# Performance work log

Measured on AMD Instinct MI355X. Metric: run time of the kernel, lower is better.

## Reference

```python
import jax, jax.numpy as jnp
import numpy as np

N_NODES = 50000
MUL_S = 256   # 0e multiplicity
MUL_V = 128   # 1o multiplicity
# combined coefficients: e3nn path_weight sqrt((2l_out+1)/fan_in) * CG normalization
C_000 = 1.0 / np.sqrt(256.0)            # 0e x 0e -> 0e
C_011 = 1.0 / np.sqrt(128.0)            # 0e x 1o -> 1o  (sqrt(3/128) * 1/sqrt(3))
C_101 = 1.0 / np.sqrt(256.0)            # 1o x 0e -> 1o
C_110 = 1.0 / np.sqrt(384.0)            # 1o x 1o -> 0e  (sqrt(1/128) * 1/sqrt(3))
C_111 = 1.0 / 16.0                      # 1o x 1o -> 1e  (sqrt(3/128) * 1/sqrt(6))

_e = np.zeros((3, 3, 3), dtype=np.float32)
_e[0, 1, 2] = _e[1, 2, 0] = _e[2, 0, 1] = 1.0
_e[0, 2, 1] = _e[2, 1, 0] = _e[1, 0, 2] = -1.0
EPS = jnp.asarray(_e)


def setup_inputs() -> dict:
    key = jax.random.key(0)
    ks = jax.random.split(key, 9)
    return {
        "node_feat": jax.random.normal(ks[0], (N_NODES, MUL_S + 3 * MUL_V), jnp.float32),
        # TensorProduct 'uvu' internal weights, one (mul_u, mul_v) matrix per path
        "w_00_0": jax.random.normal(ks[1], (MUL_S, MUL_S), jnp.float32),
        "w_01_1": jax.random.normal(ks[2], (MUL_S, MUL_V), jnp.float32),
        "w_10_1": jax.random.normal(ks[3], (MUL_V, MUL_S), jnp.float32),
        "w_11_0": jax.random.normal(ks[4], (MUL_V, MUL_V), jnp.float32),
        "w_11_1": jax.random.normal(ks[5], (MUL_V, MUL_V), jnp.float32),
        # o3.Linear weights per output irrep (fan_in, mul_out)
        "W_0e": jax.random.normal(ks[6], (MUL_S + MUL_V, MUL_S), jnp.float32),
        "W_1o": jax.random.normal(ks[7], (MUL_S + MUL_V, MUL_V), jnp.float32),
        "W_1e": jax.random.normal(ks[8], (MUL_V, MUL_V), jnp.float32),
    }


def reference(node_feat, w_00_0, w_01_1, w_10_1, w_11_0, w_11_1, W_0e, W_1o, W_1e):
    N = node_feat.shape[0]
    s = node_feat[:, :MUL_S]                                   # [N, 256]   0e
    v = node_feat[:, MUL_S:].reshape(N, MUL_V, 3)              # [N, 128, 3] 1o

    # TensorProduct paths ('uvu': out mul = mul of input-1 channel u)
    p1 = C_000 * jnp.einsum('uv,zu,zv->zu', w_00_0, s, s)          # [N,256] 0e
    p2 = C_011 * jnp.einsum('uv,zu,zvj->zuj', w_01_1, s, v)        # [N,256,3] 1o
    p3 = C_101 * jnp.einsum('uv,zuj,zv->zuj', w_10_1, v, s)        # [N,128,3] 1o
    p4 = C_110 * jnp.einsum('uv,zuj,zvj->zu', w_11_0, v, v)        # [N,128] 0e
    p5 = C_111 * jnp.einsum('uv,ijk,zui,zvj->zuk', w_11_1, EPS, v, v)  # [N,128,3] 1e

    # o3.Linear (irrep-wise mixing, 1/sqrt(fan_in) normalization)
    tp_0e = jnp.concatenate([p1, p4], axis=1)                      # [N, 384]
    tp_1o = jnp.concatenate([p2, p3], axis=1)                      # [N, 384, 3]
    out_0e = (tp_0e @ W_0e) / jnp.sqrt(384.0)                      # [N, 256]
    out_1o = jnp.einsum('zuj,uo->zoj', tp_1o, W_1o) / jnp.sqrt(384.0)  # [N,128,3]
    out_1e = jnp.einsum('zuj,uo->zoj', p5, W_1e) / jnp.sqrt(128.0)     # [N,128,3]

    return jnp.concatenate(
        [out_0e, out_1o.reshape(N, -1), out_1e.reshape(N, -1)], axis=1
    )  # [N, 1024] = 256x0e + 128x1o + 128x1e
```

## Files before the change

kernel.cpp:

```cpp
#include <hip/hip_runtime.h>

typedef _Float16 f16;
typedef _Float16 f16x8 __attribute__((ext_vector_type(8)));
typedef _Float16 f16x4 __attribute__((ext_vector_type(4)));
typedef float f32x4 __attribute__((ext_vector_type(4)));

#define MFMA16(a, b, c) __builtin_amdgcn_mfma_f32_16x16x32_f16(a, b, c, 0, 0, 0)

__device__ __forceinline__ void pack_one(int local, const float* __restrict__ src,
                                         f16* __restrict__ dst, int K, int R, int transpose) {
    int i = local & 7;
    int l = (local >> 3) & 63;
    int p = local >> 9;
    int rt16 = R >> 4;
    int rb = p % rt16;
    int kb = p / rt16;
    int k = kb * 32 + ((l >> 4) << 3) + i;
    int r = rb * 16 + (l & 15);
    float v = transpose ? src[k * R + r] : src[r * K + k];
    dst[local] = (f16)v;
}

__global__ void pack_weights(const float* __restrict__ w00, const float* __restrict__ w01,
                             const float* __restrict__ w10, const float* __restrict__ w110,
                             const float* __restrict__ w111, const float* __restrict__ W0e,
                             const float* __restrict__ W1o, const float* __restrict__ W1e,
                             f16* __restrict__ dst) {
    int idx = blockIdx.x * 256 + threadIdx.x;
    if (idx < 65536)        pack_one(idx,          w00,  dst,          256, 256, 0);
    else if (idx < 98304)   pack_one(idx - 65536,  w01,  dst + 65536,  128, 256, 0);
    else if (idx < 131072)  pack_one(idx - 98304,  w10,  dst + 98304,  256, 128, 0);
    else if (idx < 147456)  pack_one(idx - 131072, w110, dst + 131072, 128, 128, 0);
    else if (idx < 163840)  pack_one(idx - 147456, w111, dst + 147456, 128, 128, 0);
    else if (idx < 262144)  pack_one(idx - 163840, W0e,  dst + 163840, 384, 256, 1);
    else if (idx < 311296)  pack_one(idx - 262144, W1o,  dst + 262144, 384, 128, 1);
    else                    pack_one(idx - 311296, W1e,  dst + 311296, 128, 128, 1);
}

#define NT 32
#define S16B   0
#define VBASE(j) (16384 + (j) * 8192)
#define TB     40960
#define A3B    65536
#define MBASE(j) (TB + (j) * 8192)
#define P5BASE(j) ((j) == 0 ? A3B : (S16B + ((j) - 1) * 8192))
#define LDS_BYTES 73728

__device__ __forceinline__ f16x8 afrag(const unsigned char* lds, int base, int pitchh,
                                       int row0, int k0, int lr, int lg) {
    int row = row0 + lr;
    int off = base + row * (pitchh * 2) + (((k0 + (lg << 3)) * 2) ^ ((row & 7) << 4));
    return *(const f16x8*)(lds + off);
}
__device__ __forceinline__ f16x4 ldsv4(const unsigned char* lds, int base, int pitchh,
                                       int row, int col) {
    int off = base + row * (pitchh * 2) + ((col * 2) ^ ((row & 7) << 4));
    return *(const f16x4*)(lds + off);
}
__device__ __forceinline__ void stsv4(unsigned char* lds, int base, int pitchh,
                                      int row, int col, f16x4 v) {
    int off = base + row * (pitchh * 2) + ((col * 2) ^ ((row & 7) << 4));
    *(f16x4*)(lds + off) = v;
}
__device__ __forceinline__ void ldss(unsigned char* lds, int base, int pitchh,
                                     int row, int col, float v) {
    int off = base + row * (pitchh * 2) + ((col * 2) ^ ((row & 7) << 4));
    *(f16*)(lds + off) = (f16)v;
}
__device__ __forceinline__ f16x8 wfrag(const f16* __restrict__ panel, int rt16, int kb,
                                       int rb, int lane) {
    return *(const f16x8*)(panel + (size_t)((kb * rt16 + rb) * 512 + lane * 8));
}

__global__ __launch_bounds__(512, 2)
void node_tp(const float* __restrict__ nf, const f16* __restrict__ wp,
             float* __restrict__ out, int n_nodes) {
    __shared__ __align__(16) unsigned char lds[LDS_BYTES];
    const int tid = threadIdx.x;
    const int lane = tid & 63;
    const int wv = tid >> 6;
    const int z0 = blockIdx.x * NT;
    const int nvalid = min(NT, n_nodes - z0);
    const int lr = lane & 15;
    const int lg = lane >> 4;
    const int ng = wv >> 2;
    const int wr = wv & 3;

    const f16* w00p  = wp;
    const f16* w01p  = wp + 65536;
    const f16* w10p  = wp + 98304;
    const f16* w110p = wp + 131072;
    const f16* w111p = wp + 147456;
    const f16* W0ep  = wp + 163840;
    const f16* W1op  = wp + 262144;
    const f16* W1ep  = wp + 311296;

    const float C000 = 0.0625f;
    const float C011 = 0.08838834764831843f;
    const float C101 = 0.0625f;
    const float C110 = 0.05103103630798287f;
    const float C111 = 0.0625f;
    const float RS384 = 0.05103103630798287f;
    const float RS128 = 0.08838834764831843f;

    #pragma unroll 5
    for (int q = tid; q < NT * 160; q += 512) {
        int row = q / 160;
        int c4 = q - row * 160;
        float4 v4 = make_float4(0.f, 0.f, 0.f, 0.f);
        if (row < nvalid)
            v4 = ((const float4*)(nf + (size_t)(z0 + row) * 640))[c4];
        int c = c4 * 4;
        if (c < 256) {
            f16x4 h = {(f16)v4.x, (f16)v4.y, (f16)v4.z, (f16)v4.w};
            int off = S16B + row * 512 + ((c * 2) ^ ((row & 7) << 4));
            *(f16x4*)(lds + off) = h;
        } else {
            float vv[4] = {v4.x, v4.y, v4.z, v4.w};
            #pragma unroll
            for (int e = 0; e < 4; ++e) {
                int m = c - 256 + e;
                int u = m / 3;
                int j = m - u * 3;
                ldss(lds, VBASE(j), 128, row, u, vv[e]);
            }
        }
    }
    __syncthreads();

    {
        f32x4 acc[2][2] = {};
        f16x8 a0 = wfrag(w00p, 16, 0, 2 * wv, lane);
        f16x8 a1 = wfrag(w00p, 16, 0, 2 * wv + 1, lane);
        #pragma unroll 1
        for (int ks = 0; ks < 8; ++ks) {
            int kn = ks + 1 < 8 ? ks + 1 : ks;
            f16x8 n0 = wfrag(w00p, 16, kn, 2 * wv, lane);
            f16x8 n1 = wfrag(w00p, 16, kn, 2 * wv + 1, lane);
            #pragma unroll
            for (int nt = 0; nt < 2; ++nt) {
                f16x8 b = afrag(lds, S16B, 256, nt * 16, ks * 32, lr, lg);
                acc[0][nt] = MFMA16(a0, b, acc[0][nt]);
                acc[1][nt] = MFMA16(a1, b, acc[1][nt]);
            }
            a0 = n0; a1 = n1;
        }
        #pragma unroll
        for (int rt = 0; rt < 2; ++rt)
            #pragma unroll
            for (int nt = 0; nt < 2; ++nt) {
                int node = nt * 16 + lr;
                int u0 = wv * 32 + rt * 16 + lg * 4;
                f16x4 s4 = ldsv4(lds, S16B, 256, node, u0);
                f16x4 t4;
                #pragma unroll
                for (int r = 0; r < 4; ++r)
                    t4[r] = (f16)(C000 * (float)s4[r] * acc[rt][nt][r]);
                stsv4(lds, TB, 384, node, u0, t4);
            }
    }
    {
        f32x4 acc[3][2] = {};
        #pragma unroll
        for (int ks = 0; ks < 4; ++ks) {
            f16x8 a0 = wfrag(w110p, 8, ks, 2 * wr, lane);
            f16x8 a1 = wfrag(w110p, 8, ks, 2 * wr + 1, lane);
            #pragma unroll
            for (int j = 0; j < 3; ++j) {
                f16x8 b = afrag(lds, VBASE(j), 128, ng * 16, ks * 32, lr, lg);
                acc[j][0] = MFMA16(a0, b, acc[j][0]);
                acc[j][1] = MFMA16(a1, b, acc[j][1]);
            }
        }
        #pragma unroll
        for (int r2 = 0; r2 < 2; ++r2) {
            int node = ng * 16 + lr;
            int u0 = (2 * wr + r2) * 16 + lg * 4;
            float p4[4] = {0.f, 0.f, 0.f, 0.f};
            #pragma unroll
            for (int j = 0; j < 3; ++j) {
                f16x4 v4 = ldsv4(lds, VBASE(j), 128, node, u0);
                #pragma unroll
                for (int r = 0; r < 4; ++r)
                    p4[r] += (float)v4[r] * acc[j][r2][r];
            }
            f16x4 t4;
            #pragma unroll
            for (int r = 0; r < 4; ++r) t4[r] = (f16)(C110 * p4[r]);
            stsv4(lds, TB, 384, node, 256 + u0, t4);
        }
    }
    __syncthreads();

    {
        f32x4 acc[2][2] = {};
        f16x8 a0 = wfrag(W0ep, 16, 0, 2 * wv, lane);
        f16x8 a1 = wfrag(W0ep, 16, 0, 2 * wv + 1, lane);
        #pragma unroll 1
        for (int ks = 0; ks < 12; ++ks) {
            int kn = ks + 1 < 12 ? ks + 1 : ks;
            f16x8 n0 = wfrag(W0ep, 16, kn, 2 * wv, lane);
            f16x8 n1 = wfrag(W0ep, 16, kn, 2 * wv + 1, lane);
            #pragma unroll
            for (int nt = 0; nt < 2; ++nt) {
                f16x8 b = afrag(lds, TB, 384, nt * 16, ks * 32, lr, lg);
                acc[0][nt] = MFMA16(a0, b, acc[0][nt]);
                acc[1][nt] = MFMA16(a1, b, acc[1][nt]);
            }
            a0 = n0; a1 = n1;
        }
        #pragma unroll
        for (int rt = 0; rt < 2; ++rt)
            #pragma unroll
            for (int nt = 0; nt < 2; ++nt) {
                int node = nt * 16 + lr;
                if (node < nvalid) {
                    int o = wv * 32 + rt * 16 + lg * 4;
                    float4 o4;
                    o4.x = RS384 * acc[rt][nt][0];
                    o4.y = RS384 * acc[rt][nt][1];
                    o4.z = RS384 * acc[rt][nt][2];
                    o4.w = RS384 * acc[rt][nt][3];
                    *(float4*)(&out[(size_t)(z0 + node) * 1024 + o]) = o4;
                }
            }
    }
    {
        f32x4 acc[2] = {};
        f16x8 a0 = wfrag(w10p, 8, 0, 2 * wr, lane);
        f16x8 a1 = wfrag(w10p, 8, 0, 2 * wr + 1, lane);
        #pragma unroll 1
        for (int ks = 0; ks < 8; ++ks) {
            int kn = ks + 1 < 8 ? ks + 1 : ks;
            f16x8 n0 = wfrag(w10p, 8, kn, 2 * wr, lane);
            f16x8 n1 = wfrag(w10p, 8, kn, 2 * wr + 1, lane);
            f16x8 b = afrag(lds, S16B, 256, ng * 16, ks * 32, lr, lg);
            acc[0] = MFMA16(a0, b, acc[0]);
            acc[1] = MFMA16(a1, b, acc[1]);
            a0 = n0; a1 = n1;
        }
        #pragma unroll
        for (int r2 = 0; r2 < 2; ++r2) {
            int node = ng * 16 + lr;
            f16x4 t4;
            #pragma unroll
            for (int r = 0; r < 4; ++r) t4[r] = (f16)acc[r2][r];
            stsv4(lds, A3B, 128, node, (2 * wr + r2) * 16 + lg * 4, t4);
        }
    }
    __syncthreads();

    f32x4 acc1o[2][3] = {};
    #pragma unroll
    for (int j = 0; j < 3; ++j) {
        {
            f32x4 a2[2][2] = {};
            #pragma unroll
            for (int ks = 0; ks < 4; ++ks) {
                f16x8 a0 = wfrag(w01p, 16, ks, 2 * wv, lane);
                f16x8 a1 = wfrag(w01p, 16, ks, 2 * wv + 1, lane);
                #pragma unroll
                for (int nt = 0; nt < 2; ++nt) {
                    f16x8 b = afrag(lds, VBASE(j), 128, nt * 16, ks * 32, lr, lg);
                    a2[0][nt] = MFMA16(a0, b, a2[0][nt]);
                    a2[1][nt] = MFMA16(a1, b, a2[1][nt]);
                }
            }
            #pragma unroll
            for (int rt = 0; rt < 2; ++rt)
                #pragma unroll
                for (int nt = 0; nt < 2; ++nt) {
                    int node = nt * 16 + lr;
                    int u0 = wv * 32 + rt * 16 + lg * 4;
                    f16x4 s4 = ldsv4(lds, S16B, 256, node, u0);
                    f16x4 t4;
                    #pragma unroll
                    for (int r = 0; r < 4; ++r)
                        t4[r] = (f16)(C011 * (float)s4[r] * a2[rt][nt][r]);
                    stsv4(lds, TB, 384, node, u0, t4);
                }
        }
        #pragma unroll 1
        for (int q = tid; q < NT * 32; q += 512) {
            int row = q >> 5;
            int col = (q & 31) * 4;
            f16x4 v4 = ldsv4(lds, VBASE(j), 128, row, col);
            f16x4 a34 = ldsv4(lds, A3B, 128, row, col);
            f16x4 t4;
            #pragma unroll
            for (int r = 0; r < 4; ++r)
                t4[r] = (f16)(C101 * (float)v4[r] * (float)a34[r]);
            stsv4(lds, TB, 384, row, 256 + col, t4);
        }
        __syncthreads();
        {
            f16x8 a0 = wfrag(W1op, 8, 0, 2 * wr, lane);
            f16x8 a1 = wfrag(W1op, 8, 0, 2 * wr + 1, lane);
            #pragma unroll 1
            for (int ks = 0; ks < 12; ++ks) {
                int kn = ks + 1 < 12 ? ks + 1 : ks;
                f16x8 n0 = wfrag(W1op, 8, kn, 2 * wr, lane);
                f16x8 n1 = wfrag(W1op, 8, kn, 2 * wr + 1, lane);
                f16x8 b = afrag(lds, TB, 384, ng * 16, ks * 32, lr, lg);
                acc1o[0][j] = MFMA16(a0, b, acc1o[0][j]);
                acc1o[1][j] = MFMA16(a1, b, acc1o[1][j]);
                a0 = n0; a1 = n1;
            }
        }
        __syncthreads();
    }
    #pragma unroll
    for (int r2 = 0; r2 < 2; ++r2) {
        int node = ng * 16 + lr;
        if (node < nvalid) {
            int o0 = (2 * wr + r2) * 16 + lg * 4;
            float vals[12];
            #pragma unroll
            for (int r = 0; r < 4; ++r)
                #pragma unroll
                for (int j = 0; j < 3; ++j)
                    vals[r * 3 + j] = RS384 * acc1o[r2][j][r];
            size_t base = (size_t)(z0 + node) * 1024 + 256 + 3 * o0;
            #pragma unroll
            for (int qq = 0; qq < 3; ++qq) {
                float4 f;
                f.x = vals[qq * 4 + 0]; f.y = vals[qq * 4 + 1];
                f.z = vals[qq * 4 + 2]; f.w = vals[qq * 4 + 3];
                *(float4*)(&out[base + qq * 4]) = f;
            }
        }
    }

    #pragma unroll 1
    for (int j = 0; j < 3; ++j) {
        f32x4 am[2] = {};
        #pragma unroll
        for (int ks = 0; ks < 4; ++ks) {
            f16x8 a0 = wfrag(w111p, 8, ks, 2 * wr, lane);
            f16x8 a1 = wfrag(w111p, 8, ks, 2 * wr + 1, lane);
            f16x8 b = afrag(lds, VBASE(j), 128, ng * 16, ks * 32, lr, lg);
            am[0] = MFMA16(a0, b, am[0]);
            am[1] = MFMA16(a1, b, am[1]);
        }
        #pragma unroll
        for (int r2 = 0; r2 < 2; ++r2) {
            int node = ng * 16 + lr;
            f16x4 t4;
            #pragma unroll
            for (int r = 0; r < 4; ++r) t4[r] = (f16)am[r2][r];
            stsv4(lds, MBASE(j), 128, node, (2 * wr + r2) * 16 + lg * 4, t4);
        }
    }
    __syncthreads();
    #pragma unroll 1
    for (int q = tid; q < NT * 32; q += 512) {
        int row = q >> 5;
        int col = (q & 31) * 4;
        f16x4 v0 = ldsv4(lds, VBASE(0), 128, row, col);
        f16x4 v1 = ldsv4(lds, VBASE(1), 128, row, col);
        f16x4 v2 = ldsv4(lds, VBASE(2), 128, row, col);
        f16x4 m0 = ldsv4(lds, MBASE(0), 128, row, col);
        f16x4 m1 = ldsv4(lds, MBASE(1), 128, row, col);
        f16x4 m2 = ldsv4(lds, MBASE(2), 128, row, col);
        f16x4 c0, c1, c2;
        #pragma unroll
        for (int r = 0; r < 4; ++r) {
            c0[r] = (f16)(C111 * ((float)v1[r] * (float)m2[r] - (float)v2[r] * (float)m1[r]));
            c1[r] = (f16)(C111 * ((float)v2[r] * (float)m0[r] - (float)v0[r] * (float)m2[r]));
            c2[r] = (f16)(C111 * ((float)v0[r] * (float)m1[r] - (float)v1[r] * (float)m0[r]));
        }
        stsv4(lds, P5BASE(0), 128, row, col, c0);
        stsv4(lds, P5BASE(1), 128, row, col, c1);
        stsv4(lds, P5BASE(2), 128, row, col, c2);
    }
    __syncthreads();

    {
        f32x4 acc[2][3] = {};
        #pragma unroll
        for (int j = 0; j < 3; ++j)
            #pragma unroll
            for (int ks = 0; ks < 4; ++ks) {
                f16x8 a0 = wfrag(W1ep, 8, ks, 2 * wr, lane);
                f16x8 a1 = wfrag(W1ep, 8, ks, 2 * wr + 1, lane);
                f16x8 b = afrag(lds, P5BASE(j), 128, ng * 16, ks * 32, lr, lg);
                acc[0][j] = MFMA16(a0, b, acc[0][j]);
                acc[1][j] = MFMA16(a1, b, acc[1][j]);
            }
        #pragma unroll
        for (int r2 = 0; r2 < 2; ++r2) {
            int node = ng * 16 + lr;
            if (node < nvalid) {
                int o0 = (2 * wr + r2) * 16 + lg * 4;
                float vals[12];
                #pragma unroll
                for (int r = 0; r < 4; ++r)
                    #pragma unroll
                    for (int j = 0; j < 3; ++j)
                        vals[r * 3 + j] = RS128 * acc[r2][j][r];
                size_t base = (size_t)(z0 + node) * 1024 + 640 + 3 * o0;
                #pragma unroll
                for (int qq = 0; qq < 3; ++qq) {
                    float4 f;
                    f.x = vals[qq * 4 + 0]; f.y = vals[qq * 4 + 1];
                    f.z = vals[qq * 4 + 2]; f.w = vals[qq * 4 + 3];
                    *(float4*)(&out[base + qq * 4]) = f;
                }
            }
        }
    }
}

extern "C" void kernel_launch(void* const* d_in, const int* in_sizes, int n_in,
                              void* d_out, int out_size, void* d_ws, size_t ws_size,
                              hipStream_t stream) {
    const float* nf   = (const float*)d_in[0];
    const float* w00  = (const float*)d_in[1];
    const float* w01  = (const float*)d_in[2];
    const float* w10  = (const float*)d_in[3];
    const float* w110 = (const float*)d_in[4];
    const float* w111 = (const float*)d_in[5];
    const float* W0e  = (const float*)d_in[6];
    const float* W1o  = (const float*)d_in[7];
    const float* W1e  = (const float*)d_in[8];
    f16* wpack = (f16*)d_ws;

    int n_nodes = in_sizes[0] / 640;
    pack_weights<<<1280, 256, 0, stream>>>(w00, w01, w10, w110, w111, W0e, W1o, W1e, wpack);
    int blocks = (n_nodes + NT - 1) / NT;
    node_tp<<<blocks, 512, 0, stream>>>(nf, wpack, (float*)d_out, n_nodes);
}
```

Before: 194.2 us.

## Fuse w00/w10 GEMMs, keep scalar tiles in registers, shrink LDS footprint

```diff
diff --git a/kernel.cpp b/kernel.cpp
--- a/kernel.cpp
+++ b/kernel.cpp
@@ -38,13 +38,11 @@
 }
 
 #define NT 32
-#define S16B   0
-#define VBASE(j) (16384 + (j) * 8192)
-#define TB     40960
-#define A3B    65536
-#define MBASE(j) (TB + (j) * 8192)
-#define P5BASE(j) ((j) == 0 ? A3B : (S16B + ((j) - 1) * 8192))
-#define LDS_BYTES 73728
+#define ST     0
+#define VB(j)  (16384 + (j) * 8192)
+#define T2B    40960
+#define MB(j)  ((j) == 2 ? T2B : (ST + (j) * 8192))
+#define LDS_BYTES 49152
 
 __device__ __forceinline__ f16x8 afrag(const unsigned char* lds, int base, int pitchh,
                                        int row0, int k0, int lr, int lg) {
@@ -113,7 +111,7 @@
         int c = c4 * 4;
         if (c < 256) {
             f16x4 h = {(f16)v4.x, (f16)v4.y, (f16)v4.z, (f16)v4.w};
-            int off = S16B + row * 512 + ((c * 2) ^ ((row & 7) << 4));
+            int off = ST + row * 512 + ((c * 2) ^ ((row & 7) << 4));
             *(f16x4*)(lds + off) = h;
         } else {
             float vv[4] = {v4.x, v4.y, v4.z, v4.w};
@@ -122,92 +120,97 @@
                 int m = c - 256 + e;
                 int u = m / 3;
                 int j = m - u * 3;
-                ldss(lds, VBASE(j), 128, row, u, vv[e]);
-            }
-        }
-    }
+                ldss(lds, VB(j), 128, row, u, vv[e]);
+            }
+        }
+    }
+    f16x4 s4r[2][2];
+    #pragma unroll
+    for (int rt = 0; rt < 2; ++rt)
+        #pragma unroll
+        for (int nt = 0; nt < 2; ++nt) {
+            int node = nt * 16 + lr;
+            float4 f = make_float4(0.f, 0.f, 0.f, 0.f);
+            if (node < nvalid)
+                f = *(const float4*)(nf + (size_t)(z0 + node) * 640 + wv * 32 + rt * 16 + lg * 4);
+            s4r[rt][nt] = f16x4{(f16)f.x, (f16)f.y, (f16)f.z, (f16)f.w};
+        }
+    __syncthreads();
+
+    f32x4 acc1[2][2] = {};
+    f32x4 acc3[2] = {};
+    {
+        #pragma unroll
+        for (int ks = 0; ks < 8; ++ks) {
+            f16x8 a0 = wfrag(w00p, 16, ks, 2 * wv, lane);
+            f16x8 a1 = wfrag(w00p, 16, ks, 2 * wv + 1, lane);
+            f16x8 g0 = wfrag(w10p, 8, ks, 2 * wr, lane);
+            f16x8 g1 = wfrag(w10p, 8, ks, 2 * wr + 1, lane);
+            f16x8 b0 = afrag(lds, ST, 256, 0, ks * 32, lr, lg);
+            f16x8 b1 = afrag(lds, ST, 256, 16, ks * 32, lr, lg);
+            acc1[0][0] = MFMA16(a0, b0, acc1[0][0]);
+            acc1[0][1] = MFMA16(a0, b1, acc1[0][1]);
+            acc1[1][0] = MFMA16(a1, b0, acc1[1][0]);
+            acc1[1][1] = MFMA16(a1, b1, acc1[1][1]);
+            f16x8 bg = ng ? b1 : b0;
+            acc3[0] = MFMA16(g0, bg, acc3[0]);
+            acc3[1] = MFMA16(g1, bg, acc3[1]);
+        }
+        f32x4 p4p[2] = {};
+        #pragma unroll
+        for (int j = 0; j < 3; ++j) {
+            f32x4 a4[2] = {};
+            #pragma unroll
+            for (int ks = 0; ks < 4; ++ks) {
+                f16x8 h0 = wfrag(w110p, 8, ks, 2 * wr, lane);
+                f16x8 h1 = wfrag(w110p, 8, ks, 2 * wr + 1, lane);
+                f16x8 b = afrag(lds, VB(j), 128, ng * 16, ks * 32, lr, lg);
+                a4[0] = MFMA16(h0, b, a4[0]);
+                a4[1] = MFMA16(h1, b, a4[1]);
+            }
+            #pragma unroll
+            for (int r2 = 0; r2 < 2; ++r2) {
+                f16x4 v4 = ldsv4(lds, VB(j), 128, ng * 16 + lr, (2 * wr + r2) * 16 + lg * 4);
+                #pragma unroll
+                for (int r = 0; r < 4; ++r)
+                    p4p[r2][r] += (float)v4[r] * a4[r2][r];
+            }
+        }
+        #pragma unroll
+        for (int r2 = 0; r2 < 2; ++r2) {
+            f16x4 t4;
+            #pragma unroll
+            for (int r = 0; r < 4; ++r) t4[r] = (f16)(C110 * p4p[r2][r]);
+            stsv4(lds, T2B, 128, ng * 16 + lr, (2 * wr + r2) * 16 + lg * 4, t4);
+        }
+    }
+    __syncthreads();
+
+    #pragma unroll
+    for (int rt = 0; rt < 2; ++rt)
+        #pragma unroll
+        for (int nt = 0; nt < 2; ++nt) {
+            f16x4 t4;
+            #pragma unroll
+            for (int r = 0; r < 4; ++r)
+                t4[r] = (f16)(C000 * (float)s4r[rt][nt][r] * acc1[rt][nt][r]);
+            stsv4(lds, ST, 256, nt * 16 + lr, wv * 32 + rt * 16 + lg * 4, t4);
+        }
     __syncthreads();
 
     {
         f32x4 acc[2][2] = {};
-        f16x8 a0 = wfrag(w00p, 16, 0, 2 * wv, lane);
-        f16x8 a1 = wfrag(w00p, 16, 0, 2 * wv + 1, lane);
-        #pragma unroll 1
-        for (int ks = 0; ks < 8; ++ks) {
-            int kn = ks + 1 < 8 ? ks + 1 : ks;
-            f16x8 n0 = wfrag(w00p, 16, kn, 2 * wv, lane);
-            f16x8 n1 = wfrag(w00p, 16, kn, 2 * wv + 1, lane);
+        #pragma unroll
+        for (int ks = 0; ks < 12; ++ks) {
+            f16x8 a0 = wfrag(W0ep, 16, ks, 2 * wv, lane);
+            f16x8 a1 = wfrag(W0ep, 16, ks, 2 * wv + 1, lane);
             #pragma unroll
             for (int nt = 0; nt < 2; ++nt) {
-                f16x8 b = afrag(lds, S16B, 256, nt * 16, ks * 32, lr, lg);
+                f16x8 b = (ks < 8) ? afrag(lds, ST, 256, nt * 16, ks * 32, lr, lg)
+                                   : afrag(lds, T2B, 128, nt * 16, (ks - 8) * 32, lr, lg);
                 acc[0][nt] = MFMA16(a0, b, acc[0][nt]);
                 acc[1][nt] = MFMA16(a1, b, acc[1][nt]);
             }
-            a0 = n0; a1 = n1;
-        }
-        #pragma unroll
-        for (int rt = 0; rt < 2; ++rt)
-            #pragma unroll
-            for (int nt = 0; nt < 2; ++nt) {
-                int node = nt * 16 + lr;
-                int u0 = wv * 32 + rt * 16 + lg * 4;
-                f16x4 s4 = ldsv4(lds, S16B, 256, node, u0);
-                f16x4 t4;
-                #pragma unroll
-                for (int r = 0; r < 4; ++r)
-                    t4[r] = (f16)(C000 * (float)s4[r] * acc[rt][nt][r]);
-                stsv4(lds, TB, 384, node, u0, t4);
-            }
-    }
-    {
-        f32x4 acc[3][2] = {};
-        #pragma unroll
-        for (int ks = 0; ks < 4; ++ks) {
-            f16x8 a0 = wfrag(w110p, 8, ks, 2 * wr, lane);
-            f16x8 a1 = wfrag(w110p, 8, ks, 2 * wr + 1, lane);
-            #pragma unroll
-            for (int j = 0; j < 3; ++j) {
-                f16x8 b = afrag(lds, VBASE(j), 128, ng * 16, ks * 32, lr, lg);
-                acc[j][0] = MFMA16(a0, b, acc[j][0]);
-                acc[j][1] = MFMA16(a1, b, acc[j][1]);
-            }
-        }
-        #pragma unroll
-        for (int r2 = 0; r2 < 2; ++r2) {
-            int node = ng * 16 + lr;
-            int u0 = (2 * wr + r2) * 16 + lg * 4;
-            float p4[4] = {0.f, 0.f, 0.f, 0.f};
-            #pragma unroll
-            for (int j = 0; j < 3; ++j) {
-                f16x4 v4 = ldsv4(lds, VBASE(j), 128, node, u0);
-                #pragma unroll
-                for (int r = 0; r < 4; ++r)
-                    p4[r] += (float)v4[r] * acc[j][r2][r];
-            }
-            f16x4 t4;
-            #pragma unroll
-            for (int r = 0; r < 4; ++r) t4[r] = (f16)(C110 * p4[r]);
-            stsv4(lds, TB, 384, node, 256 + u0, t4);
-        }
-    }
-    __syncthreads();
-
-    {
-        f32x4 acc[2][2] = {};
-        f16x8 a0 = wfrag(W0ep, 16, 0, 2 * wv, lane);
-        f16x8 a1 = wfrag(W0ep, 16, 0, 2 * wv + 1, lane);
-        #pragma unroll 1
-        for (int ks = 0; ks < 12; ++ks) {
-            int kn = ks + 1 < 12 ? ks + 1 : ks;
-            f16x8 n0 = wfrag(W0ep, 16, kn, 2 * wv, lane);
-            f16x8 n1 = wfrag(W0ep, 16, kn, 2 * wv + 1, lane);
-            #pragma unroll
-            for (int nt = 0; nt < 2; ++nt) {
-                f16x8 b = afrag(lds, TB, 384, nt * 16, ks * 32, lr, lg);
-                acc[0][nt] = MFMA16(a0, b, acc[0][nt]);
-                acc[1][nt] = MFMA16(a1, b, acc[1][nt]);
-            }
-            a0 = n0; a1 = n1;
         }
         #pragma unroll
         for (int rt = 0; rt < 2; ++rt)
@@ -225,90 +228,55 @@
                 }
             }
     }
-    {
-        f32x4 acc[2] = {};
-        f16x8 a0 = wfrag(w10p, 8, 0, 2 * wr, lane);
-        f16x8 a1 = wfrag(w10p, 8, 0, 2 * wr + 1, lane);
-        #pragma unroll 1
-        for (int ks = 0; ks < 8; ++ks) {
-            int kn = ks + 1 < 8 ? ks + 1 : ks;
-            f16x8 n0 = wfrag(w10p, 8, kn, 2 * wr, lane);
-            f16x8 n1 = wfrag(w10p, 8, kn, 2 * wr + 1, lane);
-            f16x8 b = afrag(lds, S16B, 256, ng * 16, ks * 32, lr, lg);
-            acc[0] = MFMA16(a0, b, acc[0]);
-            acc[1] = MFMA16(a1, b, acc[1]);
-            a0 = n0; a1 = n1;
-        }
-        #pragma unroll
-        for (int r2 = 0; r2 < 2; ++r2) {
-            int node = ng * 16 + lr;
-            f16x4 t4;
-            #pragma unroll
-            for (int r = 0; r < 4; ++r) t4[r] = (f16)acc[r2][r];
-            stsv4(lds, A3B, 128, node, (2 * wr + r2) * 16 + lg * 4, t4);
-        }
-    }
-    __syncthreads();
 
     f32x4 acc1o[2][3] = {};
     #pragma unroll
     for (int j = 0; j < 3; ++j) {
-        {
-            f32x4 a2[2][2] = {};
-            #pragma unroll
-            for (int ks = 0; ks < 4; ++ks) {
-                f16x8 a0 = wfrag(w01p, 16, ks, 2 * wv, lane);
-                f16x8 a1 = wfrag(w01p, 16, ks, 2 * wv + 1, lane);
+        f32x4 acc2[2][2] = {};
+        #pragma unroll
+        for (int ks = 0; ks < 4; ++ks) {
+            f16x8 a0 = wfrag(w01p, 16, ks, 2 * wv, lane);
+            f16x8 a1 = wfrag(w01p, 16, ks, 2 * wv + 1, lane);
+            #pragma unroll
+            for (int nt = 0; nt < 2; ++nt) {
+                f16x8 b = afrag(lds, VB(j), 128, nt * 16, ks * 32, lr, lg);
+                acc2[0][nt] = MFMA16(a0, b, acc2[0][nt]);
+                acc2[1][nt] = MFMA16(a1, b, acc2[1][nt]);
+            }
+        }
+        __syncthreads();
+        #pragma unroll
+        for (int rt = 0; rt < 2; ++rt)
+            #pragma unroll
+            for (int nt = 0; nt < 2; ++nt) {
+                f16x4 t4;
                 #pragma unroll
-                for (int nt = 0; nt < 2; ++nt) {
-                    f16x8 b = afrag(lds, VBASE(j), 128, nt * 16, ks * 32, lr, lg);
-                    a2[0][nt] = MFMA16(a0, b, a2[0][nt]);
-                    a2[1][nt] = MFMA16(a1, b, a2[1][nt]);
-                }
-            }
-            #pragma unroll
-            for (int rt = 0; rt < 2; ++rt)
-                #pragma unroll
-                for (int nt = 0; nt < 2; ++nt) {
-                    int node = nt * 16 + lr;
-                    int u0 = wv * 32 + rt * 16 + lg * 4;
-                    f16x4 s4 = ldsv4(lds, S16B, 256, node, u0);
-                    f16x4 t4;
-                    #pragma unroll
-                    for (int r = 0; r < 4; ++r)
-                        t4[r] = (f16)(C011 * (float)s4[r] * a2[rt][nt][r]);
-                    stsv4(lds, TB, 384, node, u0, t4);
-                }
-        }
-        #pragma unroll 1
-        for (int q = tid; q < NT * 32; q += 512) {
-            int row = q >> 5;
-            int col = (q & 31) * 4;
-            f16x4 v4 = ldsv4(lds, VBASE(j), 128, row, col);
-            f16x4 a34 = ldsv4(lds, A3B, 128, row, col);
+                for (int r = 0; r < 4; ++r)
+                    t4[r] = (f16)(C011 * (float)s4r[rt][nt][r] * acc2[rt][nt][r]);
+                stsv4(lds, ST, 256, nt * 16 + lr, wv * 32 + rt * 16 + lg * 4, t4);
+            }
+        #pragma unroll
+        for (int r2 = 0; r2 < 2; ++r2) {
+            f16x4 v4 = ldsv4(lds, VB(j), 128, ng * 16 + lr, (2 * wr + r2) * 16 + lg * 4);
             f16x4 t4;
             #pragma unroll
             for (int r = 0; r < 4; ++r)
-                t4[r] = (f16)(C101 * (float)v4[r] * (float)a34[r]);
-            stsv4(lds, TB, 384, row, 256 + col, t4);
+                t4[r] = (f16)(C101 * (float)v4[r] * acc3[r2][r]);
+            stsv4(lds, T2B, 128, ng * 16 + lr, (2 * wr + r2) * 16 + lg * 4, t4);
         }
         __syncthreads();
-        {
-            f16x8 a0 = wfrag(W1op, 8, 0, 2 * wr, lane);
-            f16x8 a1 = wfrag(W1op, 8, 0, 2 * wr + 1, lane);
-            #pragma unroll 1
-            for (int ks = 0; ks < 12; ++ks) {
-                int kn = ks + 1 < 12 ? ks + 1 : ks;
-                f16x8 n0 = wfrag(W1op, 8, kn, 2 * wr, lane);
-                f16x8 n1 = wfrag(W1op, 8, kn, 2 * wr + 1, lane);
-                f16x8 b = afrag(lds, TB, 384, ng * 16, ks * 32, lr, lg);
-                acc1o[0][j] = MFMA16(a0, b, acc1o[0][j]);
-                acc1o[1][j] = MFMA16(a1, b, acc1o[1][j]);
-                a0 = n0; a1 = n1;
-            }
-        }
-        __syncthreads();
-    }
+        #pragma unroll
+        for (int ks = 0; ks < 12; ++ks) {
+            f16x8 a0 = wfrag(W1op, 8, ks, 2 * wr, lane);
+            f16x8 a1 = wfrag(W1op, 8, ks, 2 * wr + 1, lane);
+            f16x8 b = (ks < 8) ? afrag(lds, ST, 256, ng * 16, ks * 32, lr, lg)
+                               : afrag(lds, T2B, 128, ng * 16, (ks - 8) * 32, lr, lg);
+            acc1o[0][j] = MFMA16(a0, b, acc1o[0][j]);
+            acc1o[1][j] = MFMA16(a1, b, acc1o[1][j]);
+        }
+    }
+    __syncthreads();
+
     #pragma unroll
     for (int r2 = 0; r2 < 2; ++r2) {
         int node = ng * 16 + lr;
@@ -331,37 +299,37 @@
         }
     }
 
-    #pragma unroll 1
+    #pragma unroll
     for (int j = 0; j < 3; ++j) {
         f32x4 am[2] = {};
         #pragma unroll
         for (int ks = 0; ks < 4; ++ks) {
-            f16x8 a0 = wfrag(w111p, 8, ks, 2 * wr, lane);
-            f16x8 a1 = wfrag(w111p, 8, ks, 2 * wr + 1, lane);
-            f16x8 b = afrag(lds, VBASE(j), 128, ng * 16, ks * 32, lr, lg);
-            am[0] = MFMA16(a0, b, am[0]);
-            am[1] = MFMA16(a1, b, am[1]);
+            f16x8 h0 = wfrag(w111p, 8, ks, 2 * wr, lane);
+            f16x8 h1 = wfrag(w111p, 8, ks, 2 * wr + 1, lane);
+            f16x8 b = afrag(lds, VB(j), 128, ng * 16, ks * 32, lr, lg);
+            am[0] = MFMA16(h0, b, am[0]);
+            am[1] = MFMA16(h1, b, am[1]);
         }
         #pragma unroll
         for (int r2 = 0; r2 < 2; ++r2) {
-            int node = ng * 16 + lr;
             f16x4 t4;
             #pragma unroll
             for (int r = 0; r < 4; ++r) t4[r] = (f16)am[r2][r];
-            stsv4(lds, MBASE(j), 128, node, (2 * wr + r2) * 16 + lg * 4, t4);
-        }
-    }
-    __syncthreads();
+            stsv4(lds, MB(j), 128, ng * 16 + lr, (2 * wr + r2) * 16 + lg * 4, t4);
+        }
+    }
+    __syncthreads();
+
     #pragma unroll 1
     for (int q = tid; q < NT * 32; q += 512) {
         int row = q >> 5;
         int col = (q & 31) * 4;
-        f16x4 v0 = ldsv4(lds, VBASE(0), 128, row, col);
-        f16x4 v1 = ldsv4(lds, VBASE(1), 128, row, col);
-        f16x4 v2 = ldsv4(lds, VBASE(2), 128, row, col);
-        f16x4 m0 = ldsv4(lds, MBASE(0), 128, row, col);
-        f16x4 m1 = ldsv4(lds, MBASE(1), 128, row, col);
-        f16x4 m2 = ldsv4(lds, MBASE(2), 128, row, col);
+        f16x4 v0 = ldsv4(lds, VB(0), 128, row, col);
+        f16x4 v1 = ldsv4(lds, VB(1), 128, row, col);
+        f16x4 v2 = ldsv4(lds, VB(2), 128, row, col);
+        f16x4 m0 = ldsv4(lds, MB(0), 128, row, col);
+        f16x4 m1 = ldsv4(lds, MB(1), 128, row, col);
+        f16x4 m2 = ldsv4(lds, MB(2), 128, row, col);
         f16x4 c0, c1, c2;
         #pragma unroll
         for (int r = 0; r < 4; ++r) {
@@ -369,9 +337,9 @@
             c1[r] = (f16)(C111 * ((float)v2[r] * (float)m0[r] - (float)v0[r] * (float)m2[r]));
             c2[r] = (f16)(C111 * ((float)v0[r] * (float)m1[r] - (float)v1[r] * (float)m0[r]));
         }
-        stsv4(lds, P5BASE(0), 128, row, col, c0);
-        stsv4(lds, P5BASE(1), 128, row, col, c1);
-        stsv4(lds, P5BASE(2), 128, row, col, c2);
+        stsv4(lds, VB(0), 128, row, col, c0);
+        stsv4(lds, VB(1), 128, row, col, c1);
+        stsv4(lds, VB(2), 128, row, col, c2);
     }
     __syncthreads();
 
@@ -383,7 +351,7 @@
             for (int ks = 0; ks < 4; ++ks) {
                 f16x8 a0 = wfrag(W1ep, 8, ks, 2 * wr, lane);
                 f16x8 a1 = wfrag(W1ep, 8, ks, 2 * wr + 1, lane);
-                f16x8 b = afrag(lds, P5BASE(j), 128, ng * 16, ks * 32, lr, lg);
+                f16x8 b = afrag(lds, VB(j), 128, ng * 16, ks * 32, lr, lg);
                 acc[0][j] = MFMA16(a0, b, acc[0][j]);
                 acc[1][j] = MFMA16(a1, b, acc[1][j]);
             }
```

Measured after the change: 261.8 us. 34.8% more time.

## Shrink LDS footprint by keeping TP intermediates in registers and reusing buffers

Applied to the files above, without the earlier changes.

```diff
diff --git a/kernel.cpp b/kernel.cpp
--- a/kernel.cpp
+++ b/kernel.cpp
@@ -6,6 +6,11 @@
 typedef float f32x4 __attribute__((ext_vector_type(4)));
 
 #define MFMA16(a, b, c) __builtin_amdgcn_mfma_f32_16x16x32_f16(a, b, c, 0, 0, 0)
+
+__device__ __forceinline__ void barrier_lds() {
+    asm volatile("s_waitcnt lgkmcnt(0)" ::: "memory");
+    __builtin_amdgcn_s_barrier();
+}
 
 __device__ __forceinline__ void pack_one(int local, const float* __restrict__ src,
                                          f16* __restrict__ dst, int K, int R, int transpose) {
@@ -38,13 +43,11 @@
 }
 
 #define NT 32
-#define S16B   0
-#define VBASE(j) (16384 + (j) * 8192)
-#define TB     40960
-#define A3B    65536
-#define MBASE(j) (TB + (j) * 8192)
-#define P5BASE(j) ((j) == 0 ? A3B : (S16B + ((j) - 1) * 8192))
-#define LDS_BYTES 73728
+#define STA    0
+#define VB(j)  (16384 + (j) * 8192)
+#define T2B    40960
+#define MB(j)  ((j) == 2 ? T2B : (STA + (j) * 8192))
+#define LDS_BYTES 49152
 
 __device__ __forceinline__ f16x8 afrag(const unsigned char* lds, int base, int pitchh,
                                        int row0, int k0, int lr, int lg) {
@@ -72,7 +75,7 @@
     return *(const f16x8*)(panel + (size_t)((kb * rt16 + rb) * 512 + lane * 8));
 }
 
-__global__ __launch_bounds__(512, 2)
+__global__ __launch_bounds__(512, 6)
 void node_tp(const float* __restrict__ nf, const f16* __restrict__ wp,
              float* __restrict__ out, int n_nodes) {
     __shared__ __align__(16) unsigned char lds[LDS_BYTES];
@@ -113,7 +116,7 @@
         int c = c4 * 4;
         if (c < 256) {
             f16x4 h = {(f16)v4.x, (f16)v4.y, (f16)v4.z, (f16)v4.w};
-            int off = S16B + row * 512 + ((c * 2) ^ ((row & 7) << 4));
+            int off = STA + row * 512 + ((c * 2) ^ ((row & 7) << 4));
             *(f16x4*)(lds + off) = h;
         } else {
             float vv[4] = {v4.x, v4.y, v4.z, v4.w};
@@ -122,14 +125,25 @@
                 int m = c - 256 + e;
                 int u = m / 3;
                 int j = m - u * 3;
-                ldss(lds, VBASE(j), 128, row, u, vv[e]);
-            }
-        }
-    }
-    __syncthreads();
-
+                ldss(lds, VB(j), 128, row, u, vv[e]);
+            }
+        }
+    }
+    f16x4 s4r[2][2];
+    #pragma unroll
+    for (int rt = 0; rt < 2; ++rt)
+        #pragma unroll
+        for (int nt = 0; nt < 2; ++nt) {
+            int node = nt * 16 + lr;
+            float4 f = make_float4(0.f, 0.f, 0.f, 0.f);
+            if (node < nvalid)
+                f = *(const float4*)(nf + (size_t)(z0 + node) * 640 + wv * 32 + rt * 16 + lg * 4);
+            s4r[rt][nt] = f16x4{(f16)f.x, (f16)f.y, (f16)f.z, (f16)f.w};
+        }
+    barrier_lds();
+
+    f32x4 acc1[2][2] = {};
     {
-        f32x4 acc[2][2] = {};
         f16x8 a0 = wfrag(w00p, 16, 0, 2 * wv, lane);
         f16x8 a1 = wfrag(w00p, 16, 0, 2 * wv + 1, lane);
         #pragma unroll 1
@@ -139,37 +153,39 @@
             f16x8 n1 = wfrag(w00p, 16, kn, 2 * wv + 1, lane);
             #pragma unroll
             for (int nt = 0; nt < 2; ++nt) {
-                f16x8 b = afrag(lds, S16B, 256, nt * 16, ks * 32, lr, lg);
-                acc[0][nt] = MFMA16(a0, b, acc[0][nt]);
-                acc[1][nt] = MFMA16(a1, b, acc[1][nt]);
+                f16x8 b = afrag(lds, STA, 256, nt * 16, ks * 32, lr, lg);
+                acc1[0][nt] = MFMA16(a0, b, acc1[0][nt]);
+                acc1[1][nt] = MFMA16(a1, b, acc1[1][nt]);
             }
             a0 = n0; a1 = n1;
         }
-        #pragma unroll
-        for (int rt = 0; rt < 2; ++rt)
-            #pragma unroll
-            for (int nt = 0; nt < 2; ++nt) {
-                int node = nt * 16 + lr;
-                int u0 = wv * 32 + rt * 16 + lg * 4;
-                f16x4 s4 = ldsv4(lds, S16B, 256, node, u0);
-                f16x4 t4;
-                #pragma unroll
-                for (int r = 0; r < 4; ++r)
-                    t4[r] = (f16)(C000 * (float)s4[r] * acc[rt][nt][r]);
-                stsv4(lds, TB, 384, node, u0, t4);
-            }
-    }
+    }
+    f32x4 acc3[2] = {};
     {
-        f32x4 acc[3][2] = {};
+        f16x8 a0 = wfrag(w10p, 8, 0, 2 * wr, lane);
+        f16x8 a1 = wfrag(w10p, 8, 0, 2 * wr + 1, lane);
+        #pragma unroll 1
+        for (int ks = 0; ks < 8; ++ks) {
+            int kn = ks + 1 < 8 ? ks + 1 : ks;
+            f16x8 n0 = wfrag(w10p, 8, kn, 2 * wr, lane);
+            f16x8 n1 = wfrag(w10p, 8, kn, 2 * wr + 1, lane);
+            f16x8 b = afrag(lds, STA, 256, ng * 16, ks * 32, lr, lg);
+            acc3[0] = MFMA16(a0, b, acc3[0]);
+            acc3[1] = MFMA16(a1, b, acc3[1]);
+            a0 = n0; a1 = n1;
+        }
+    }
+    {
+        f32x4 a4[3][2] = {};
         #pragma unroll
         for (int ks = 0; ks < 4; ++ks) {
             f16x8 a0 = wfrag(w110p, 8, ks, 2 * wr, lane);
             f16x8 a1 = wfrag(w110p, 8, ks, 2 * wr + 1, lane);
             #pragma unroll
             for (int j = 0; j < 3; ++j) {
-                f16x8 b = afrag(lds, VBASE(j), 128, ng * 16, ks * 32, lr, lg);
-                acc[j][0] = MFMA16(a0, b, acc[j][0]);
-                acc[j][1] = MFMA16(a1, b, acc[j][1]);
+                f16x8 b = afrag(lds, VB(j), 128, ng * 16, ks * 32, lr, lg);
+                a4[j][0] = MFMA16(a0, b, a4[j][0]);
+                a4[j][1] = MFMA16(a1, b, a4[j][1]);
             }
         }
         #pragma unroll
@@ -179,18 +195,30 @@
             float p4[4] = {0.f, 0.f, 0.f, 0.f};
             #pragma unroll
             for (int j = 0; j < 3; ++j) {
-                f16x4 v4 = ldsv4(lds, VBASE(j), 128, node, u0);
+                f16x4 v4 = ldsv4(lds, VB(j), 128, node, u0);
                 #pragma unroll
                 for (int r = 0; r < 4; ++r)
-                    p4[r] += (float)v4[r] * acc[j][r2][r];
+                    p4[r] += (float)v4[r] * a4[j][r2][r];
             }
             f16x4 t4;
             #pragma unroll
             for (int r = 0; r < 4; ++r) t4[r] = (f16)(C110 * p4[r]);
-            stsv4(lds, TB, 384, node, 256 + u0, t4);
-        }
-    }
-    __syncthreads();
+            stsv4(lds, T2B, 128, node, u0, t4);
+        }
+    }
+    barrier_lds();
+
+    #pragma unroll
+    for (int rt = 0; rt < 2; ++rt)
+        #pragma unroll
+        for (int nt = 0; nt < 2; ++nt) {
+            f16x4 t4;
+            #pragma unroll
+            for (int r = 0; r < 4; ++r)
+                t4[r] = (f16)(C000 * (float)s4r[rt][nt][r] * acc1[rt][nt][r]);
+            stsv4(lds, STA, 256, nt * 16 + lr, wv * 32 + rt * 16 + lg * 4, t4);
+        }
+    barrier_lds();
 
     {
         f32x4 acc[2][2] = {};
@@ -203,7 +231,8 @@
             f16x8 n1 = wfrag(W0ep, 16, kn, 2 * wv + 1, lane);
             #pragma unroll
             for (int nt = 0; nt < 2; ++nt) {
-                f16x8 b = afrag(lds, TB, 384, nt * 16, ks * 32, lr, lg);
+                f16x8 b = (ks < 8) ? afrag(lds, STA, 256, nt * 16, ks * 32, lr, lg)
+                                   : afrag(lds, T2B, 128, nt * 16, (ks - 8) * 32, lr, lg);
                 acc[0][nt] = MFMA16(a0, b, acc[0][nt]);
                 acc[1][nt] = MFMA16(a1, b, acc[1][nt]);
             }
@@ -225,74 +254,43 @@
                 }
             }
     }
-    {
-        f32x4 acc[2] = {};
-        f16x8 a0 = wfrag(w10p, 8, 0, 2 * wr, lane);
-        f16x8 a1 = wfrag(w10p, 8, 0, 2 * wr + 1, lane);
-        #pragma unroll 1
-        for (int ks = 0; ks < 8; ++ks) {
-            int kn = ks + 1 < 8 ? ks + 1 : ks;
-            f16x8 n0 = wfrag(w10p, 8, kn, 2 * wr, lane);
-            f16x8 n1 = wfrag(w10p, 8, kn, 2 * wr + 1, lane);
-            f16x8 b = afrag(lds, S16B, 256, ng * 16, ks * 32, lr, lg);
-            acc[0] = MFMA16(a0, b, acc[0]);
-            acc[1] = MFMA16(a1, b, acc[1]);
-            a0 = n0; a1 = n1;
-        }
-        #pragma unroll
-        for (int r2 = 0; r2 < 2; ++r2) {
-            int node = ng * 16 + lr;
-            f16x4 t4;
-            #pragma unroll
-            for (int r = 0; r < 4; ++r) t4[r] = (f16)acc[r2][r];
-            stsv4(lds, A3B, 128, node, (2 * wr + r2) * 16 + lg * 4, t4);
-        }
-    }
-    __syncthreads();
 
     f32x4 acc1o[2][3] = {};
     #pragma unroll
     for (int j = 0; j < 3; ++j) {
-        {
-            f32x4 a2[2][2] = {};
-            #pragma unroll
-            for (int ks = 0; ks < 4; ++ks) {
-                f16x8 a0 = wfrag(w01p, 16, ks, 2 * wv, lane);
-                f16x8 a1 = wfrag(w01p, 16, ks, 2 * wv + 1, lane);
+        f32x4 a2[2][2] = {};
+        #pragma unroll
+        for (int ks = 0; ks < 4; ++ks) {
+            f16x8 a0 = wfrag(w01p, 16, ks, 2 * wv, lane);
+            f16x8 a1 = wfrag(w01p, 16, ks, 2 * wv + 1, lane);
+            #pragma unroll
+            for (int nt = 0; nt < 2; ++nt) {
+                f16x8 b = afrag(lds, VB(j), 128, nt * 16, ks * 32, lr, lg);
+                a2[0][nt] = MFMA16(a0, b, a2[0][nt]);
+                a2[1][nt] = MFMA16(a1, b, a2[1][nt]);
+            }
+        }
+        barrier_lds();
+        #pragma unroll
+        for (int rt = 0; rt < 2; ++rt)
+            #pragma unroll
+            for (int nt = 0; nt < 2; ++nt) {
+                f16x4 t4;
                 #pragma unroll
-                for (int nt = 0; nt < 2; ++nt) {
-                    f16x8 b = afrag(lds, VBASE(j), 128, nt * 16, ks * 32, lr, lg);
-                    a2[0][nt] = MFMA16(a0, b, a2[0][nt]);
-                    a2[1][nt] = MFMA16(a1, b, a2[1][nt]);
-                }
-            }
-            #pragma unroll
-            for (int rt = 0; rt < 2; ++rt)
-                #pragma unroll
-                for (int nt = 0; nt < 2; ++nt) {
-                    int node = nt * 16 + lr;
-                    int u0 = wv * 32 + rt * 16 + lg * 4;
-                    f16x4 s4 = ldsv4(lds, S16B, 256, node, u0);
-                    f16x4 t4;
-                    #pragma unroll
-                    for (int r = 0; r < 4; ++r)
-                        t4[r] = (f16)(C011 * (float)s4[r] * a2[rt][nt][r]);
-                    stsv4(lds, TB, 384, node, u0, t4);
-                }
-        }
-        #pragma unroll 1
-        for (int q = tid; q < NT * 32; q += 512) {
-            int row = q >> 5;
-            int col = (q & 31) * 4;
-            f16x4 v4 = ldsv4(lds, VBASE(j), 128, row, col);
-            f16x4 a34 = ldsv4(lds, A3B, 128, row, col);
+                for (int r = 0; r < 4; ++r)
+                    t4[r] = (f16)(C011 * (float)s4r[rt][nt][r] * a2[rt][nt][r]);
+                stsv4(lds, STA, 256, nt * 16 + lr, wv * 32 + rt * 16 + lg * 4, t4);
+            }
+        #pragma unroll
+        for (int r2 = 0; r2 < 2; ++r2) {
+            f16x4 v4 = ldsv4(lds, VB(j), 128, ng * 16 + lr, (2 * wr + r2) * 16 + lg * 4);
             f16x4 t4;
             #pragma unroll
             for (int r = 0; r < 4; ++r)
-                t4[r] = (f16)(C101 * (float)v4[r] * (float)a34[r]);
-            stsv4(lds, TB, 384, row, 256 + col, t4);
-        }
-        __syncthreads();
+                t4[r] = (f16)(C101 * (float)v4[r] * acc3[r2][r]);
+            stsv4(lds, T2B, 128, ng * 16 + lr, (2 * wr + r2) * 16 + lg * 4, t4);
+        }
+        barrier_lds();
         {
             f16x8 a0 = wfrag(W1op, 8, 0, 2 * wr, lane);
             f16x8 a1 = wfrag(W1op, 8, 0, 2 * wr + 1, lane);
@@ -301,14 +299,16 @@
                 int kn = ks + 1 < 12 ? ks + 1 : ks;
                 f16x8 n0 = wfrag(W1op, 8, kn, 2 * wr, lane);
                 f16x8 n1 = wfrag(W1op, 8, kn, 2 * wr + 1, lane);
-                f16x8 b = afrag(lds, TB, 384, ng * 16, ks * 32, lr, lg);
+                f16x8 b = (ks < 8) ? afrag(lds, STA, 256, ng * 16, ks * 32, lr, lg)
+                                   : afrag(lds, T2B, 128, ng * 16, (ks - 8) * 32, lr, lg);
                 acc1o[0][j] = MFMA16(a0, b, acc1o[0][j]);
                 acc1o[1][j] = MFMA16(a1, b, acc1o[1][j]);
                 a0 = n0; a1 = n1;
             }
         }
-        __syncthreads();
-    }
+    }
+    barrier_lds();
+
     #pragma unroll
     for (int r2 = 0; r2 < 2; ++r2) {
         int node = ng * 16 + lr;
@@ -331,37 +331,37 @@
         }
     }
 
-    #pragma unroll 1
+    #pragma unroll
     for (int j = 0; j < 3; ++j) {
         f32x4 am[2] = {};
         #pragma unroll
         for (int ks = 0; ks < 4; ++ks) {
             f16x8 a0 = wfrag(w111p, 8, ks, 2 * wr, lane);
             f16x8 a1 = wfrag(w111p, 8, ks, 2 * wr + 1, lane);
-            f16x8 b = afrag(lds, VBASE(j), 128, ng * 16, ks * 32, lr, lg);
+            f16x8 b = afrag(lds, VB(j), 128, ng * 16, ks * 32, lr, lg);
             am[0] = MFMA16(a0, b, am[0]);
             am[1] = MFMA16(a1, b, am[1]);
         }
         #pragma unroll
         for (int r2 = 0; r2 < 2; ++r2) {
-            int node = ng * 16 + lr;
             f16x4 t4;
             #pragma unroll
             for (int r = 0; r < 4; ++r) t4[r] = (f16)am[r2][r];
-            stsv4(lds, MBASE(j), 128, node, (2 * wr + r2) * 16 + lg * 4, t4);
-        }
-    }
-    __syncthreads();
+            stsv4(lds, MB(j), 128, ng * 16 + lr, (2 * wr + r2) * 16 + lg * 4, t4);
+        }
+    }
+    barrier_lds();
+
     #pragma unroll 1
     for (int q = tid; q < NT * 32; q += 512) {
         int row = q >> 5;
         int col = (q & 31) * 4;
-        f16x4 v0 = ldsv4(lds, VBASE(0), 128, row, col);
-        f16x4 v1 = ldsv4(lds, VBASE(1), 128, row, col);
-        f16x4 v2 = ldsv4(lds, VBASE(2), 128, row, col);
-        f16x4 m0 = ldsv4(lds, MBASE(0), 128, row, col);
-        f16x4 m1 = ldsv4(lds, MBASE(1), 128, row, col);
-        f16x4 m2 = ldsv4(lds, MBASE(2), 128, row, col);
+        f16x4 v0 = ldsv4(lds, VB(0), 128, row, col);
+        f16x4 v1 = ldsv4(lds, VB(1), 128, row, col);
+        f16x4 v2 = ldsv4(lds, VB(2), 128, row, col);
+        f16x4 m0 = ldsv4(lds, MB(0), 128, row, col);
+        f16x4 m1 = ldsv4(lds, MB(1), 128, row, col);
+        f16x4 m2 = ldsv4(lds, MB(2), 128, row, col);
         f16x4 c0, c1, c2;
         #pragma unroll
         for (int r = 0; r < 4; ++r) {
@@ -369,11 +369,11 @@
             c1[r] = (f16)(C111 * ((float)v2[r] * (float)m0[r] - (float)v0[r] * (float)m2[r]));
             c2[r] = (f16)(C111 * ((float)v0[r] * (float)m1[r] - (float)v1[r] * (float)m0[r]));
         }
-        stsv4(lds, P5BASE(0), 128, row, col, c0);
-        stsv4(lds, P5BASE(1), 128, row, col, c1);
-        stsv4(lds, P5BASE(2), 128, row, col, c2);
-    }
-    __syncthreads();
+        stsv4(lds, VB(0), 128, row, col, c0);
+        stsv4(lds, VB(1), 128, row, col, c1);
+        stsv4(lds, VB(2), 128, row, col, c2);
+    }
+    barrier_lds();
 
     {
         f32x4 acc[2][3] = {};
@@ -383,7 +383,7 @@
             for (int ks = 0; ks < 4; ++ks) {
                 f16x8 a0 = wfrag(W1ep, 8, ks, 2 * wr, lane);
                 f16x8 a1 = wfrag(W1ep, 8, ks, 2 * wr + 1, lane);
-                f16x8 b = afrag(lds, P5BASE(j), 128, ng * 16, ks * 32, lr, lg);
+                f16x8 b = afrag(lds, VB(j), 128, ng * 16, ks * 32, lr, lg);
                 acc[0][j] = MFMA16(a0, b, acc[0][j]);
                 acc[1][j] = MFMA16(a1, b, acc[1][j]);
             }
```

Measured after the change: 265.7 us. +36.8%, slower.
